# Kernel tuning notes

Hardware: AMD Instinct MI355X
Metric: run time of the kernel (lower is better)

Reference implementation:

```python
import jax, jax.numpy as jnp
import numpy as np

N_HEADS = 16


def setup_inputs() -> dict:
    key = jax.random.key(0)
    ks = jax.random.split(key, 6)
    b, s, d = 1, 2048, 2048
    x = jax.random.normal(ks[0], (b, s, d), dtype=jnp.float32)
    Wqkv = jax.random.normal(ks[1], (d, 3 * d), dtype=jnp.float32) * (d ** -0.5)
    Wqkv_bias = jax.random.normal(ks[2], (3 * d,), dtype=jnp.float32) * 0.02
    out_w = jax.random.normal(ks[3], (d, d), dtype=jnp.float32) * (d ** -0.5)
    out_b = jax.random.normal(ks[4], (d,), dtype=jnp.float32) * 0.02
    attn_bias = jax.random.normal(ks[5], (1, N_HEADS, 1, s), dtype=jnp.float32)
    key_padding_mask = jnp.ones((b, s), dtype=bool)
    return {"x": x, "Wqkv": Wqkv, "Wqkv_bias": Wqkv_bias, "out_w": out_w,
            "out_b": out_b, "attn_bias": attn_bias,
            "key_padding_mask": key_padding_mask}


def reference(x, Wqkv, Wqkv_bias, out_w, out_b, attn_bias, key_padding_mask):
    b, s, d = x.shape
    h = N_HEADS
    dh = d // h
    qkv = x @ Wqkv + Wqkv_bias                      # [b, s, 3d]
    q, k, v = jnp.split(qkv, 3, axis=-1)
    q = q.reshape(b, s, h, dh).transpose(0, 2, 1, 3)  # b h s d
    k = k.reshape(b, s, h, dh).transpose(0, 2, 1, 3)
    v = v.reshape(b, s, h, dh).transpose(0, 2, 1, 3)
    scale = 1.0 / jnp.sqrt(jnp.asarray(dh, x.dtype))
    attn_weight = jnp.einsum('bhqd,bhkd->bhqk', q, k) * scale
    attn_weight = attn_weight + attn_bias           # broadcast [1,h,1,s]
    min_val = jnp.finfo(x.dtype).min
    # key padding mask: [b, s_k] -> [b,1,1,s_k]
    attn_weight = jnp.where(key_padding_mask[:, None, None, :], attn_weight, min_val)
    # causal mask (s_q == s_k)
    causal = jnp.tril(jnp.ones((s, s), dtype=bool))
    attn_weight = jnp.where(causal[None, None, :, :], attn_weight, min_val)
    attn_weight = jax.nn.softmax(attn_weight, axis=-1)
    out = jnp.einsum('bhqk,bhkd->bhqd', attn_weight, v)
    out = out.transpose(0, 2, 1, 3).reshape(b, s, d)  # b s (h d)
    return out @ out_w + out_b
```

## Files before the change

### kernel.cpp

```cpp
#include <hip/hip_runtime.h>
#include <hip/hip_bf16.h>
#include <stdint.h>


#define SQ 2048
#define DM 2048
#define NH 16
#define DH 128
#define N3 6144
#define QKVN (NH * SQ * DH)

typedef unsigned short u16;
typedef __bf16 bf16_t;
typedef bf16_t bf16x8 __attribute__((ext_vector_type(8)));
typedef float f32x4 __attribute__((ext_vector_type(4)));
typedef const __attribute__((address_space(1))) unsigned int guint;
typedef __attribute__((address_space(3))) unsigned int luint;

__device__ __forceinline__ float b2f(u16 u) {
    union { uint32_t i; float f; } c; c.i = ((uint32_t)u) << 16; return c.f;
}
__device__ __forceinline__ u16 f2b(float f) {
    union { float f; uint32_t i; } c; c.f = f;
    uint32_t r = c.i + 0x7FFF + ((c.i >> 16) & 1);
    return (u16)(r >> 16);
}
__device__ __forceinline__ uint32_t pk(u16 a, u16 b) {
    return (uint32_t)a | ((uint32_t)b << 16);
}
__device__ __forceinline__ uint32_t pkrnd(float a, float b) {
    union { float f; uint32_t i; } x, y; x.f = a; y.f = b;
    return __builtin_amdgcn_perm(y.i + 0x8000u, x.i + 0x8000u, 0x07060302u);
}
__device__ __forceinline__ float ld1(const void* p, size_t i, bool fp32) {
    return fp32 ? ((const float*)p)[i] : b2f(((const u16*)p)[i]);
}

__global__ void detect_dtype(const void* x, int* flag) {
    __shared__ int bad;
    if (threadIdx.x == 0) bad = 0;
    __syncthreads();
    float v = b2f(((const u16*)x)[threadIdx.x]);
    if (!(fabsf(v) <= 1024.0f)) atomicOr(&bad, 1);
    __syncthreads();
    if (threadIdx.x == 0) *flag = bad;
}

__global__ __launch_bounds__(256) void convert_x(
    const void* __restrict__ x, u16* __restrict__ xb, const int* __restrict__ flagp)
{
    const bool fp32 = (*flagp != 0);
    const size_t i = ((size_t)blockIdx.x * 256 + threadIdx.x) * 8;
    uint4 v;
    if (fp32) {
        const float* p = (const float*)x + i;
        float4 a = *(const float4*)p, b = *(const float4*)(p + 4);
        v.x = pkrnd(a.x, a.y); v.y = pkrnd(a.z, a.w);
        v.z = pkrnd(b.x, b.y); v.w = pkrnd(b.z, b.w);
    } else {
        v = *(const uint4*)((const u16*)x + i);
    }
    *(uint4*)(xb + i) = v;
}

__global__ __launch_bounds__(256) void transpose_w(
    const void* __restrict__ W, u16* __restrict__ Wt, int N,
    const int* __restrict__ flagp)
{
    const bool fp32 = (*flagp != 0);
    __shared__ __attribute__((aligned(16))) u16 tile[64 * 72];
    const int t = threadIdx.x;
    const int n0 = blockIdx.x * 64, k0 = blockIdx.y * 64;
#pragma unroll
    for (int i = 0; i < 2; ++i) {
        int c = t + 256 * i; int kr = c >> 3; int n8 = (c & 7) * 8;
        uint4 v;
        if (fp32) {
            const float* p = (const float*)W + (size_t)(k0 + kr) * N + n0 + n8;
            float4 a = *(const float4*)p, b = *(const float4*)(p + 4);
            v.x = pkrnd(a.x, a.y); v.y = pkrnd(a.z, a.w);
            v.z = pkrnd(b.x, b.y); v.w = pkrnd(b.z, b.w);
        } else {
            v = *(const uint4*)((const u16*)W + (size_t)(k0 + kr) * N + n0 + n8);
        }
        *(uint4*)&tile[kr * 72 + n8] = v;
    }
    __syncthreads();
#pragma unroll
    for (int i = 0; i < 2; ++i) {
        int c = t + 256 * i; int nr = c >> 3; int k8 = (c & 7) * 8;
        uint32_t dw[4];
#pragma unroll
        for (int j = 0; j < 4; ++j)
            dw[j] = pk(tile[(k8 + 2*j) * 72 + nr], tile[(k8 + 2*j + 1) * 72 + nr]);
        *(uint4*)&Wt[(size_t)(n0 + nr) * 2048 + k0 + k8] =
            make_uint4(dw[0], dw[1], dw[2], dw[3]);
    }
}

__global__ __launch_bounds__(256, 2) void qkv_gemm4(
    const u16* __restrict__ xb, const u16* __restrict__ Wt,
    const void* __restrict__ bias,
    u16* __restrict__ Q, u16* __restrict__ K, u16* __restrict__ Vt,
    const int* __restrict__ flagp)
{
    const bool fp32 = (*flagp != 0);
    __shared__ __attribute__((aligned(16))) u16 Alds[2][128 * 64];
    __shared__ __attribute__((aligned(16))) u16 Blds[2][192 * 64];
    const int t = threadIdx.x;
    const int w = t >> 6, l = t & 63;
    const int wm = w >> 1, wn = w & 1;
    const int lq = l & 15, quad = l >> 4;
    const int rsub = t >> 3;
    const int sw = ((t & 7) ^ (rsub & 7)) << 3;

    const int orig = blockIdx.x;
    const int xcd = orig & 7, j = orig >> 3;
    const int bx = (xcd & 3) * 8 + (j & 7);
    const int by = (xcd >> 2) * 8 + (j >> 3);
    const int m0 = by * 128, n0 = bx * 192;

    const u16* Ag = xb + (size_t)m0 * 2048;
    const u16* Bg = Wt + (size_t)n0 * 2048;

#define STAGE_A(u) do {                                                       \
    if ((u) < 32) {                                                           \
      _Pragma("unroll")                                                       \
      for (int i_ = 0; i_ < 4; ++i_) {                                        \
        const int rb_ = i_ * 32;                                              \
        const u16* src_ = Ag + (size_t)(rb_ + rsub) * 2048 + (u) * 64 + sw;   \
        __builtin_amdgcn_global_load_lds((guint*)(const void*)src_,           \
          (luint*)(void*)&Alds[(u) & 1][rb_ * 64 + t * 8], 16, 0, 0);         \
      }                                                                       \
    } } while (0)

#define STAGE_B(u) do {                                                       \
    if ((u) < 32) {                                                           \
      _Pragma("unroll")                                                       \
      for (int i_ = 0; i_ < 6; ++i_) {                                        \
        const int rb_ = i_ * 32;                                              \
        const u16* src_ = Bg + (size_t)(rb_ + rsub) * 2048 + (u) * 64 + sw;   \
        __builtin_amdgcn_global_load_lds((guint*)(const void*)src_,           \
          (luint*)(void*)&Blds[(u) & 1][rb_ * 64 + t * 8], 16, 0, 0);         \
      }                                                                       \
    } } while (0)

#define READ_A(buf, mh) do {                                                  \
    _Pragma("unroll")                                                         \
    for (int mf_ = 0; mf_ < 2; ++mf_) {                                       \
      const int r_ = wm*64 + ((mh)*2 + mf_)*16 + lq;                          \
      _Pragma("unroll")                                                       \
      for (int ks_ = 0; ks_ < 2; ++ks_) {                                     \
        const int c_ = (ks_*4 + quad) ^ (r_ & 7);                             \
        a[(mh)*2 + mf_][ks_] = *(const bf16x8*)&Alds[buf][r_*64 + c_*8];      \
      }                                                                       \
    } } while (0)

#define READ_B(dst, buf, nhh) do {                                            \
    _Pragma("unroll")                                                         \
    for (int nf_ = 0; nf_ < 3; ++nf_) {                                       \
      const int r_ = wn*96 + ((nhh)*3 + nf_)*16 + lq;                         \
      _Pragma("unroll")                                                       \
      for (int ks_ = 0; ks_ < 2; ++ks_) {                                     \
        const int c_ = (ks_*4 + quad) ^ (r_ & 7);                             \
        dst[nf_][ks_] = *(const bf16x8*)&Blds[buf][r_*64 + c_*8];             \
      }                                                                       \
    } } while (0)

#define MMA_Q(mh, nhh, bsrc) do {                                             \
    _Pragma("unroll")                                                         \
    for (int mf_ = 0; mf_ < 2; ++mf_)                                         \
    _Pragma("unroll")                                                         \
    for (int nf_ = 0; nf_ < 3; ++nf_)                                         \
    _Pragma("unroll")                                                         \
    for (int ks_ = 0; ks_ < 2; ++ks_)                                         \
      acc[(mh)*2+mf_][(nhh)*3+nf_] =                                          \
        __builtin_amdgcn_mfma_f32_16x16x32_bf16(a[(mh)*2+mf_][ks_],           \
          bsrc[nf_][ks_], acc[(mh)*2+mf_][(nhh)*3+nf_], 0, 0, 0);             \
    } while (0)

    const f32x4 vzero = {0.f, 0.f, 0.f, 0.f};
    f32x4 acc[4][6];
#pragma unroll
    for (int i = 0; i < 4; ++i)
#pragma unroll
        for (int j2 = 0; j2 < 6; ++j2) acc[i][j2] = vzero;
    bf16x8 a[4][2], b0[3][2], b1[3][2];

    STAGE_A(0); STAGE_B(0);
    asm volatile("s_waitcnt vmcnt(0)" ::: "memory");
    __builtin_amdgcn_s_barrier();

#pragma unroll 1
    for (int T = 0; T < 32; ++T) {
        const int buf = T & 1;
        STAGE_A(T + 1); STAGE_B(T + 1);
        READ_A(buf, 0); READ_A(buf, 1);
        READ_B(b0, buf, 0); READ_B(b1, buf, 1);
        asm volatile("s_waitcnt lgkmcnt(0)" ::: "memory");
        __builtin_amdgcn_s_setprio(1);
        MMA_Q(0, 0, b0); MMA_Q(0, 1, b1);
        MMA_Q(1, 0, b0); MMA_Q(1, 1, b1);
        __builtin_amdgcn_s_setprio(0);
        asm volatile("s_waitcnt vmcnt(0)" ::: "memory");
        __builtin_amdgcn_s_barrier();
    }

    const float scale = 0.08838834764831845f;
#pragma unroll
    for (int nf = 0; nf < 6; ++nf) {
        const int n = n0 + wn*96 + nf*16 + lq;
        const float bn = ld1(bias, n, fp32);
        const int which = n >> 11, r2 = n & 2047, h = r2 >> 7, dc = r2 & 127;
#pragma unroll
        for (int mf = 0; mf < 4; ++mf) {
#pragma unroll
            for (int r = 0; r < 4; ++r) {
                const int m = m0 + wm*64 + mf*16 + quad*4 + r;
                const float val = acc[mf][nf][r] + bn;
                if (which == 0)
                    Q[((size_t)(h << 11) + m) * DH + dc] = f2b(val * scale);
                else if (which == 1)
                    K[((size_t)(h << 11) + m) * DH + dc] = f2b(val);
                else {
                    const int kl = m & 63;
                    const int pos = ((kl >> 5) << 5) + (((kl >> 2) & 3) << 3)
                                  + (((kl >> 4) & 1) << 2) + (kl & 3);
                    const int mp = (m & ~63) | pos;
                    Vt[((size_t)h * DH + dc) * SQ + mp] = f2b(val);
                }
            }
        }
    }
#undef STAGE_A
#undef STAGE_B
#undef READ_A
#undef READ_B
#undef MMA_Q
}

__global__ __launch_bounds__(256) void attn_mfma(
    const u16* __restrict__ Q, const u16* __restrict__ K,
    const u16* __restrict__ Vt, const void* __restrict__ attn_bias,
    u16* __restrict__ Ob0, u16* __restrict__ Ob1,
    float* __restrict__ Lb0, float* __restrict__ Lb1,
    const int* __restrict__ flagp)
{
    const bool fp32 = (*flagp != 0);
    __shared__ __attribute__((aligned(16))) u16 Ks[2][4 * 64 * 32];
    __shared__ __attribute__((aligned(16))) u16 Vs[2][128 * 64];
    __shared__ __attribute__((aligned(16))) float biasF[2048];

    const int t = threadIdx.x;
    const int w = t >> 6, l = t & 63;
    const int lq = l & 15, quad = l >> 4;
    const int px = blockIdx.x, h = blockIdx.y, par = blockIdx.z;

    const u16* Qh = Q + (size_t)h * SQ * DH;
    const u16* Kh = K + (size_t)h * SQ * DH;
    const u16* Vh = Vt + (size_t)h * DH * SQ;
    u16* Ob = par ? Ob1 : Ob0;
    float* Lb = par ? Lb1 : Lb0;

#pragma unroll
    for (int i = 0; i < 8; ++i) {
        int j = t + 256 * i;
        biasF[j] = ld1(attn_bias, (size_t)h * SQ + j, fp32);
    }

#define STAGE_KV(kt_, b_) do {                                                \
    const int k0_ = (kt_) * 64;                                               \
    _Pragma("unroll")                                                         \
    for (int i_ = 0; i_ < 4; ++i_) {                                          \
        const int ci_ = w * 4 + i_;                                           \
        const int kc_ = ci_ >> 2, kg_ = ci_ & 3;                              \
        const u16* srck_ = Kh + (size_t)(k0_ + kg_*16 + (l >> 2)) * DH        \
                         + kc_*32 + (l & 3) * 8;                              \
        __builtin_amdgcn_global_load_lds((guint*)(const void*)srck_,          \
            (luint*)(void*)&Ks[b_][ci_ * 512], 16, 0, 0);                     \
        const int dim_ = ci_ * 8 + (l >> 3);                                  \
        const u16* srcv_ = Vh + (size_t)dim_ * SQ + k0_                       \
                         + (((l & 7) ^ (l >> 3)) << 3);                       \
        __builtin_amdgcn_global_load_lds((guint*)(const void*)srcv_,          \
            (luint*)(void*)&Vs[b_][ci_ * 512], 16, 0, 0);                     \
    } } while (0)

    const f32x4 vzero = {0.f, 0.f, 0.f, 0.f};

    for (int phase = 0; phase < 2; ++phase) {
        const int qt = phase ? (15 - px) : px;
        const int q0 = qt * 128;
        const int qb = q0 + w * 32;

        bf16x8 bq[2][4];
#pragma unroll
        for (int s = 0; s < 2; ++s)
#pragma unroll
            for (int kc = 0; kc < 4; ++kc)
                bq[s][kc] = *(const bf16x8*)(Qh + (size_t)(qb + s*16 + lq) * DH
                                             + kc*32 + quad*8);

        __syncthreads();
        STAGE_KV(par, 0);
        asm volatile("s_waitcnt vmcnt(0)" ::: "memory");
        __builtin_amdgcn_s_barrier();

        f32x4 O[2][8];
#pragma unroll
        for (int s = 0; s < 2; ++s)
#pragma unroll
            for (int i = 0; i < 8; ++i) O[s][i] = vzero;
        float lsum[2] = {0.0f, 0.0f};

        int buf = 0;
        const int ktmax = 2 * qt + 1;
        for (int kt = par; kt <= ktmax; kt += 2) {
            const int k0 = kt * 64;
            if (kt + 2 <= ktmax) STAGE_KV(kt + 2, buf ^ 1);

            f32x4 S[2][4];
#pragma unroll
            for (int s = 0; s < 2; ++s)
#pragma unroll
                for (int ks = 0; ks < 4; ++ks) S[s][ks] = vzero;
#pragma unroll
            for (int kc = 0; kc < 4; ++kc) {
#pragma unroll
                for (int ks = 0; ks < 4; ++ks) {
                    bf16x8 ak = *(const bf16x8*)&Ks[buf][kc*2048 + (ks*16 + lq)*32 + quad*8];
                    S[0][ks] = __builtin_amdgcn_mfma_f32_16x16x32_bf16(ak, bq[0][kc], S[0][ks], 0, 0, 0);
                    S[1][ks] = __builtin_amdgcn_mfma_f32_16x16x32_bf16(ak, bq[1][kc], S[1][ks], 0, 0, 0);
                }
            }

            uint32_t Ppk[2][4][2];
#pragma unroll
            for (int s = 0; s < 2; ++s) {
                const int qbs = qb + s * 16;
                const bool full = (k0 + 63) <= qbs;
                float part = 0.0f;
#pragma unroll
                for (int ks = 0; ks < 4; ++ks) {
                    const f32x4 b4 = *(const f32x4*)&biasF[k0 + ks*16 + quad*4];
                    float p[4];
#pragma unroll
                    for (int r = 0; r < 4; ++r) {
                        float pe = __expf(S[s][ks][r] + b4[r]);
                        if (!full) {
                            const int key = k0 + ks*16 + quad*4 + r;
                            if (key > qbs + lq) pe = 0.0f;
                        }
                        p[r] = pe;
                        part += pe;
                    }
                    Ppk[s][ks][0] = pkrnd(p[0], p[1]);
                    Ppk[s][ks][1] = pkrnd(p[2], p[3]);
                }
                lsum[s] += part;
            }

#pragma unroll
            for (int s2 = 0; s2 < 2; ++s2) {
                union { uint32_t u[4]; bf16x8 v; } bP0, bP1;
                bP0.u[0] = Ppk[0][2*s2][0];   bP0.u[1] = Ppk[0][2*s2][1];
                bP0.u[2] = Ppk[0][2*s2+1][0]; bP0.u[3] = Ppk[0][2*s2+1][1];
                bP1.u[0] = Ppk[1][2*s2][0];   bP1.u[1] = Ppk[1][2*s2][1];
                bP1.u[2] = Ppk[1][2*s2+1][0]; bP1.u[3] = Ppk[1][2*s2+1][1];
                const int ch = ((s2*4 + quad) ^ (lq & 7)) << 3;
#pragma unroll
                for (int ds = 0; ds < 8; ++ds) {
                    bf16x8 aV = *(const bf16x8*)&Vs[buf][(ds*16 + lq)*64 + ch];
                    O[0][ds] = __builtin_amdgcn_mfma_f32_16x16x32_bf16(aV, bP0.v, O[0][ds], 0, 0, 0);
                    O[1][ds] = __builtin_amdgcn_mfma_f32_16x16x32_bf16(aV, bP1.v, O[1][ds], 0, 0, 0);
                }
            }

            asm volatile("s_waitcnt vmcnt(0)" ::: "memory");
            __builtin_amdgcn_s_barrier();
            buf ^= 1;
        }

#pragma unroll
        for (int s = 0; s < 2; ++s) {
            float ls = lsum[s];
            ls += __shfl_xor(ls, 16, 64);
            ls += __shfl_xor(ls, 32, 64);
            if (l < 16) Lb[(size_t)h * SQ + qb + s*16 + l] = ls;
            u16* orow = Ob + (size_t)(qb + s*16 + lq) * DM + h * DH;
#pragma unroll
            for (int ds = 0; ds < 8; ++ds) {
                uint2 o2;
                o2.x = pkrnd(O[s][ds][0], O[s][ds][1]);
                o2.y = pkrnd(O[s][ds][2], O[s][ds][3]);
                *(uint2*)&orow[ds*16 + quad*4] = o2;
            }
        }
    }
#undef STAGE_KV
}

__global__ __launch_bounds__(256) void combine_o(
    const u16* __restrict__ O0, const u16* __restrict__ O1,
    const float* __restrict__ L0, const float* __restrict__ L1,
    u16* __restrict__ attno)
{
    const size_t i = ((size_t)blockIdx.x * 256 + threadIdx.x) * 8;
    const int row = (int)(i >> 11);
    const int h = ((int)i & 2047) >> 7;
    const float inv = 1.0f / (L0[h * SQ + row] + L1[h * SQ + row]);
    const ushort4 a = *(const ushort4*)(O0 + i);
    const ushort4 b = *(const ushort4*)(O1 + i);
    const ushort4 c = *(const ushort4*)(O0 + i + 4);
    const ushort4 d = *(const ushort4*)(O1 + i + 4);
    uint4 v;
    v.x = pkrnd((b2f(a.x)+b2f(b.x))*inv, (b2f(a.y)+b2f(b.y))*inv);
    v.y = pkrnd((b2f(a.z)+b2f(b.z))*inv, (b2f(a.w)+b2f(b.w))*inv);
    v.z = pkrnd((b2f(c.x)+b2f(d.x))*inv, (b2f(c.y)+b2f(d.y))*inv);
    v.w = pkrnd((b2f(c.z)+b2f(d.z))*inv, (b2f(c.w)+b2f(d.w))*inv);
    *(uint4*)(attno + i) = v;
}

__global__ __launch_bounds__(256, 2) void out_gemm(
    const u16* __restrict__ attno, const u16* __restrict__ OWt,
    const void* __restrict__ bias, void* __restrict__ out,
    const int* __restrict__ flagp)
{
    const bool fp32 = (*flagp != 0);
    __shared__ __attribute__((aligned(16))) u16 Alds[2][64 * 64];
    __shared__ __attribute__((aligned(16))) u16 Blds[2][128 * 64];
    const int t = threadIdx.x;
    const int w = t >> 6, l = t & 63;
    const int wm = w >> 1, wn = w & 1;
    const int lq = l & 15, quad = l >> 4;
    const int rsub = t >> 3;
    const int sw = ((t & 7) ^ (rsub & 7)) << 3;

    const int orig = blockIdx.x;
    const int xcd = orig & 7, j = orig >> 3;
    const int bx = (xcd & 3) * 4 + (j & 3);
    const int by = (xcd >> 2) * 16 + (j >> 2);
    const int m0 = by * 64, n0 = bx * 128;

    const u16* Ag = attno + (size_t)m0 * 2048;
    const u16* Bg = OWt + (size_t)n0 * 2048;

#define O_STAGE_A(u) do {                                                     \
    if ((u) < 32) {                                                           \
      _Pragma("unroll")                                                       \
      for (int i_ = 0; i_ < 2; ++i_) {                                        \
        const int rb_ = i_ * 32;                                              \
        const u16* src_ = Ag + (size_t)(rb_ + rsub) * 2048 + (u) * 64 + sw;   \
        __builtin_amdgcn_global_load_lds((guint*)(const void*)src_,           \
          (luint*)(void*)&Alds[(u) & 1][rb_ * 64 + t * 8], 16, 0, 0);         \
      }                                                                       \
    } } while (0)

#define O_STAGE_B(u) do {                                                     \
    if ((u) < 32) {                                                           \
      _Pragma("unroll")                                                       \
      for (int i_ = 0; i_ < 4; ++i_) {                                        \
        const int rb_ = i_ * 32;                                              \
        const u16* src_ = Bg + (size_t)(rb_ + rsub) * 2048 + (u) * 64 + sw;   \
        __builtin_amdgcn_global_load_lds((guint*)(const void*)src_,           \
          (luint*)(void*)&Blds[(u) & 1][rb_ * 64 + t * 8], 16, 0, 0);         \
      }                                                                       \
    } } while (0)

#define O_READ_A(buf, mh) do {                                                \
    const int r_ = wm*32 + (mh)*16 + lq;                                      \
    _Pragma("unroll")                                                         \
    for (int ks_ = 0; ks_ < 2; ++ks_) {                                       \
        const int c_ = (ks_*4 + quad) ^ (r_ & 7);                             \
        a[mh][ks_] = *(const bf16x8*)&Alds[buf][r_*64 + c_*8];                \
    } } while (0)

#define O_READ_B(dst, buf, nhh) do {                                          \
    _Pragma("unroll")                                                         \
    for (int nf_ = 0; nf_ < 2; ++nf_) {                                       \
      const int r_ = wn*64 + ((nhh)*2 + nf_)*16 + lq;                         \
      _Pragma("unroll")                                                       \
      for (int ks_ = 0; ks_ < 2; ++ks_) {                                     \
        const int c_ = (ks_*4 + quad) ^ (r_ & 7);                             \
        dst[nf_][ks_] = *(const bf16x8*)&Blds[buf][r_*64 + c_*8];             \
      }                                                                       \
    } } while (0)

#define O_MMA(mh, nhh, bsrc) do {                                             \
    _Pragma("unroll")                                                         \
    for (int nf_ = 0; nf_ < 2; ++nf_)                                         \
    _Pragma("unroll")                                                         \
    for (int ks_ = 0; ks_ < 2; ++ks_)                                         \
      acc[mh][(nhh)*2+nf_] =                                                  \
        __builtin_amdgcn_mfma_f32_16x16x32_bf16(a[mh][ks_], bsrc[nf_][ks_],   \
          acc[mh][(nhh)*2+nf_], 0, 0, 0);                                     \
    } while (0)

    const f32x4 vzero = {0.f, 0.f, 0.f, 0.f};
    f32x4 acc[2][4];
#pragma unroll
    for (int i = 0; i < 2; ++i)
#pragma unroll
        for (int j2 = 0; j2 < 4; ++j2) acc[i][j2] = vzero;
    bf16x8 a[2][2], b0[2][2], b1[2][2];

    O_STAGE_A(0); O_STAGE_B(0);
    asm volatile("s_waitcnt vmcnt(0)" ::: "memory");
    __builtin_amdgcn_s_barrier();

#pragma unroll 1
    for (int T = 0; T < 32; ++T) {
        const int buf = T & 1;
        O_STAGE_A(T + 1); O_STAGE_B(T + 1);
        O_READ_A(buf, 0); O_READ_A(buf, 1);
        O_READ_B(b0, buf, 0); O_READ_B(b1, buf, 1);
        asm volatile("s_waitcnt lgkmcnt(0)" ::: "memory");
        __builtin_amdgcn_s_setprio(1);
        O_MMA(0, 0, b0); O_MMA(0, 1, b1);
        O_MMA(1, 0, b0); O_MMA(1, 1, b1);
        __builtin_amdgcn_s_setprio(0);
        asm volatile("s_waitcnt vmcnt(0)" ::: "memory");
        __builtin_amdgcn_s_barrier();
    }

#pragma unroll
    for (int nf = 0; nf < 4; ++nf) {
        const int n = n0 + wn*64 + nf*16 + lq;
        const float bn = ld1(bias, n, fp32);
#pragma unroll
        for (int mh = 0; mh < 2; ++mh) {
#pragma unroll
            for (int r = 0; r < 4; ++r) {
                const int m = m0 + wm*32 + mh*16 + quad*4 + r;
                const float v = acc[mh][nf][r] + bn;
                const size_t idx = (size_t)m * DM + n;
                if (fp32) ((float*)out)[idx] = v;
                else      ((u16*)out)[idx]  = f2b(v);
            }
        }
    }
#undef O_STAGE_A
#undef O_STAGE_B
#undef O_READ_A
#undef O_READ_B
#undef O_MMA
}

extern "C" void kernel_launch(void* const* d_in, const int* in_sizes, int n_in,
                              void* d_out, int out_size, void* d_ws, size_t ws_size,
                              hipStream_t stream)
{
    const void* x      = d_in[0];
    const void* wqkv   = d_in[1];
    const void* wqkv_b = d_in[2];
    const void* out_w  = d_in[3];
    const void* out_b  = d_in[4];
    const void* attn_b = d_in[5];

    char* base = (char*)d_ws;
    int* flag = (int*)base;
    u16* xb   = (u16*)(base + 256);
    u16* Wt   = xb + (size_t)SQ * DM;
    u16* Qb   = Wt + (size_t)N3 * DM;
    u16* Kb   = Qb + QKVN;
    u16* Vtb  = Kb + QKVN;
    float* L0 = (float*)(Vtb + QKVN);
    float* L1 = L0 + NH * SQ;
    u16* OWt  = Wt;
    u16* Ob0  = Wt + (size_t)DM * DM;
    u16* Ob1  = Ob0 + (size_t)SQ * DM;
    u16* attno = xb;

    detect_dtype<<<1, 256, 0, stream>>>(x, flag);
    convert_x<<<(SQ * DM) / (256 * 8), 256, 0, stream>>>(x, xb, flag);
    transpose_w<<<dim3(N3/64, DM/64), 256, 0, stream>>>(wqkv, Wt, N3, flag);
    qkv_gemm4<<<dim3(512), 256, 0, stream>>>(xb, Wt, wqkv_b, Qb, Kb, Vtb, flag);
    transpose_w<<<dim3(DM/64, DM/64), 256, 0, stream>>>(out_w, OWt, DM, flag);
    attn_mfma<<<dim3(8, NH, 2), 256, 0, stream>>>(Qb, Kb, Vtb, attn_b,
                                                  Ob0, Ob1, L0, L1, flag);
    combine_o<<<(SQ * DM) / (256 * 8), 256, 0, stream>>>(Ob0, Ob1, L0, L1, attno);
    out_gemm<<<dim3(512), 256, 0, stream>>>(attno, OWt, out_b, d_out, flag);
}
```

Before: 283.9 us.

## Fuse prep kernels and software-pipeline the QKV GEMM with 2-deep prefetch

Merges dtype detection, x conversion and both weight transposes into one prep launch, and moves OWt to its own workspace region so the out_w transpose no longer has to wait for the QKV GEMM. The QKV GEMM main loop is restructured into four sub-phases per K-tile. Each phase interleaves LDS fragment reads, split global-to-LDS staging two tiles ahead, and MFMA bursts, using partial vmcnt waits in place of a full drain every iteration. This aims to hide global-load latency and trim launch overhead, but it adds more barriers and a larger workspace footprint.

```diff
diff --git a/kernel.cpp b/kernel.cpp
--- a/kernel.cpp
+++ b/kernel.cpp
@@ -36,50 +36,63 @@
     return fp32 ? ((const float*)p)[i] : b2f(((const u16*)p)[i]);
 }
 
-__global__ void detect_dtype(const void* x, int* flag) {
+__global__ __launch_bounds__(256) void prep(
+    const void* __restrict__ x, const void* __restrict__ wqkv,
+    const void* __restrict__ out_w,
+    u16* __restrict__ xb, u16* __restrict__ Wt, u16* __restrict__ OWt,
+    int* __restrict__ flag)
+{
     __shared__ int bad;
-    if (threadIdx.x == 0) bad = 0;
-    __syncthreads();
-    float v = b2f(((const u16*)x)[threadIdx.x]);
-    if (!(fabsf(v) <= 1024.0f)) atomicOr(&bad, 1);
-    __syncthreads();
-    if (threadIdx.x == 0) *flag = bad;
-}
-
-__global__ __launch_bounds__(256) void convert_x(
-    const void* __restrict__ x, u16* __restrict__ xb, const int* __restrict__ flagp)
-{
-    const bool fp32 = (*flagp != 0);
-    const size_t i = ((size_t)blockIdx.x * 256 + threadIdx.x) * 8;
-    uint4 v;
-    if (fp32) {
-        const float* p = (const float*)x + i;
-        float4 a = *(const float4*)p, b = *(const float4*)(p + 4);
-        v.x = pkrnd(a.x, a.y); v.y = pkrnd(a.z, a.w);
-        v.z = pkrnd(b.x, b.y); v.w = pkrnd(b.z, b.w);
-    } else {
-        v = *(const uint4*)((const u16*)x + i);
-    }
-    *(uint4*)(xb + i) = v;
-}
-
-__global__ __launch_bounds__(256) void transpose_w(
-    const void* __restrict__ W, u16* __restrict__ Wt, int N,
-    const int* __restrict__ flagp)
-{
-    const bool fp32 = (*flagp != 0);
     __shared__ __attribute__((aligned(16))) u16 tile[64 * 72];
     const int t = threadIdx.x;
-    const int n0 = blockIdx.x * 64, k0 = blockIdx.y * 64;
+    if (t == 0) bad = 0;
+    __syncthreads();
+    {
+        float v = b2f(((const u16*)x)[t]);
+        if (!(fabsf(v) <= 1024.0f)) atomicOr(&bad, 1);
+    }
+    __syncthreads();
+    const bool fp32 = (bad != 0);
+    const int b = blockIdx.x;
+    if (b == 0 && t == 0) *flag = bad;
+
+    if (b < 2048) {
+        const size_t i = ((size_t)b * 256 + t) * 8;
+        uint4 v;
+        if (fp32) {
+            const float* p = (const float*)x + i;
+            float4 a = *(const float4*)p, b4 = *(const float4*)(p + 4);
+            v.x = pkrnd(a.x, a.y);  v.y = pkrnd(a.z, a.w);
+            v.z = pkrnd(b4.x, b4.y); v.w = pkrnd(b4.z, b4.w);
+        } else {
+            v = *(const uint4*)((const u16*)x + i);
+        }
+        *(uint4*)(xb + i) = v;
+        return;
+    }
+
+    const void* W;
+    u16* dst;
+    int N, bx, by;
+    if (b < 5120) {
+        W = wqkv; dst = Wt; N = N3;
+        const int idx = b - 2048;
+        bx = idx % 96; by = idx / 96;
+    } else {
+        W = out_w; dst = OWt; N = DM;
+        const int idx = b - 5120;
+        bx = idx % 32; by = idx / 32;
+    }
+    const int n0 = bx * 64, k0 = by * 64;
 #pragma unroll
     for (int i = 0; i < 2; ++i) {
         int c = t + 256 * i; int kr = c >> 3; int n8 = (c & 7) * 8;
         uint4 v;
         if (fp32) {
             const float* p = (const float*)W + (size_t)(k0 + kr) * N + n0 + n8;
-            float4 a = *(const float4*)p, b = *(const float4*)(p + 4);
-            v.x = pkrnd(a.x, a.y); v.y = pkrnd(a.z, a.w);
-            v.z = pkrnd(b.x, b.y); v.w = pkrnd(b.z, b.w);
+            float4 a = *(const float4*)p, b4 = *(const float4*)(p + 4);
+            v.x = pkrnd(a.x, a.y);  v.y = pkrnd(a.z, a.w);
+            v.z = pkrnd(b4.x, b4.y); v.w = pkrnd(b4.z, b4.w);
         } else {
             v = *(const uint4*)((const u16*)W + (size_t)(k0 + kr) * N + n0 + n8);
         }
@@ -93,7 +106,7 @@
 #pragma unroll
         for (int j = 0; j < 4; ++j)
             dw[j] = pk(tile[(k8 + 2*j) * 72 + nr], tile[(k8 + 2*j + 1) * 72 + nr]);
-        *(uint4*)&Wt[(size_t)(n0 + nr) * 2048 + k0 + k8] =
+        *(uint4*)&dst[(size_t)(n0 + nr) * 2048 + k0 + k8] =
             make_uint4(dw[0], dw[1], dw[2], dw[3]);
     }
 }
@@ -123,11 +136,11 @@
     const u16* Ag = xb + (size_t)m0 * 2048;
     const u16* Bg = Wt + (size_t)n0 * 2048;
 
-#define STAGE_A(u) do {                                                       \
+#define STAGE_A(u, ue) do {                                                   \
     if ((u) < 32) {                                                           \
       _Pragma("unroll")                                                       \
-      for (int i_ = 0; i_ < 4; ++i_) {                                        \
-        const int rb_ = i_ * 32;                                              \
+      for (int i_ = 0; i_ < 2; ++i_) {                                        \
+        const int rb_ = i_ * 64 + (ue) * 32;                                  \
         const u16* src_ = Ag + (size_t)(rb_ + rsub) * 2048 + (u) * 64 + sw;   \
         __builtin_amdgcn_global_load_lds((guint*)(const void*)src_,           \
           (luint*)(void*)&Alds[(u) & 1][rb_ * 64 + t * 8], 16, 0, 0);         \
@@ -152,7 +165,7 @@
       _Pragma("unroll")                                                       \
       for (int ks_ = 0; ks_ < 2; ++ks_) {                                     \
         const int c_ = (ks_*4 + quad) ^ (r_ & 7);                             \
-        a[(mh)*2 + mf_][ks_] = *(const bf16x8*)&Alds[buf][r_*64 + c_*8];      \
+        a[mf_][ks_] = *(const bf16x8*)&Alds[buf][r_*64 + c_*8];               \
       }                                                                       \
     } } while (0)
 
@@ -168,6 +181,7 @@
     } } while (0)
 
 #define MMA_Q(mh, nhh, bsrc) do {                                             \
+    __builtin_amdgcn_s_setprio(1);                                            \
     _Pragma("unroll")                                                         \
     for (int mf_ = 0; mf_ < 2; ++mf_)                                         \
     _Pragma("unroll")                                                         \
@@ -175,9 +189,42 @@
     _Pragma("unroll")                                                         \
     for (int ks_ = 0; ks_ < 2; ++ks_)                                         \
       acc[(mh)*2+mf_][(nhh)*3+nf_] =                                          \
-        __builtin_amdgcn_mfma_f32_16x16x32_bf16(a[(mh)*2+mf_][ks_],           \
-          bsrc[nf_][ks_], acc[(mh)*2+mf_][(nhh)*3+nf_], 0, 0, 0);             \
-    } while (0)
+        __builtin_amdgcn_mfma_f32_16x16x32_bf16(a[mf_][ks_], bsrc[nf_][ks_],  \
+          acc[(mh)*2+mf_][(nhh)*3+nf_], 0, 0, 0);                             \
+    __builtin_amdgcn_s_setprio(0);                                            \
+} while (0)
+
+#define TILE_BODY(T, buf, BEC, BEN) do {                                      \
+                                                                      \
+    READ_A(buf, 0);                                                           \
+    __builtin_amdgcn_s_barrier();                                             \
+    asm volatile("s_waitcnt lgkmcnt(0)" ::: "memory");                        \
+    MMA_Q(0, 0, BEC);                                                         \
+    __builtin_amdgcn_s_barrier();                                             \
+                                                                      \
+    READ_B(bo, buf, 1);                                                       \
+    STAGE_A((T) + 2, 0);                                                      \
+    if ((T) >= 30) asm volatile("s_waitcnt vmcnt(0)" ::: "memory");           \
+    else           asm volatile("s_waitcnt vmcnt(2)" ::: "memory");           \
+    __builtin_amdgcn_s_barrier();                                             \
+    asm volatile("s_waitcnt lgkmcnt(0)" ::: "memory");                        \
+    MMA_Q(0, 1, bo);                                                          \
+    __builtin_amdgcn_s_barrier();                                             \
+                                                                      \
+    READ_A(buf, 1);                                                           \
+    STAGE_B((T) + 2);                                                         \
+    __builtin_amdgcn_s_barrier();                                             \
+    asm volatile("s_waitcnt lgkmcnt(0)" ::: "memory");                        \
+    MMA_Q(1, 1, bo);                                                          \
+    __builtin_amdgcn_s_barrier();                                             \
+                                                                      \
+    READ_B(BEN, (buf) ^ 1, 0);                                                \
+    STAGE_A((T) + 2, 1);                                                      \
+    __builtin_amdgcn_s_barrier();                                             \
+    asm volatile("s_waitcnt lgkmcnt(0)" ::: "memory");                        \
+    MMA_Q(1, 0, BEC);                                                         \
+    __builtin_amdgcn_s_barrier();                                             \
+} while (0)
 
     const f32x4 vzero = {0.f, 0.f, 0.f, 0.f};
     f32x4 acc[4][6];
@@ -185,25 +232,18 @@
     for (int i = 0; i < 4; ++i)
 #pragma unroll
         for (int j2 = 0; j2 < 6; ++j2) acc[i][j2] = vzero;
-    bf16x8 a[4][2], b0[3][2], b1[3][2];
-
-    STAGE_A(0); STAGE_B(0);
-    asm volatile("s_waitcnt vmcnt(0)" ::: "memory");
+    bf16x8 a[2][2], bo[3][2], be_a[3][2], be_b[3][2];
+
+    STAGE_A(0, 0); STAGE_B(0); STAGE_A(0, 1);
+    STAGE_A(1, 0); STAGE_B(1); STAGE_A(1, 1);
+    asm volatile("s_waitcnt vmcnt(10)" ::: "memory");
     __builtin_amdgcn_s_barrier();
+    READ_B(be_a, 0, 0);
 
 #pragma unroll 1
-    for (int T = 0; T < 32; ++T) {
-        const int buf = T & 1;
-        STAGE_A(T + 1); STAGE_B(T + 1);
-        READ_A(buf, 0); READ_A(buf, 1);
-        READ_B(b0, buf, 0); READ_B(b1, buf, 1);
-        asm volatile("s_waitcnt lgkmcnt(0)" ::: "memory");
-        __builtin_amdgcn_s_setprio(1);
-        MMA_Q(0, 0, b0); MMA_Q(0, 1, b1);
-        MMA_Q(1, 0, b0); MMA_Q(1, 1, b1);
-        __builtin_amdgcn_s_setprio(0);
-        asm volatile("s_waitcnt vmcnt(0)" ::: "memory");
-        __builtin_amdgcn_s_barrier();
+    for (int T = 0; T < 32; T += 2) {
+        TILE_BODY(T,     0, be_a, be_b);
+        TILE_BODY(T + 1, 1, be_b, be_a);
     }
 
     const float scale = 0.08838834764831845f;
@@ -237,6 +277,7 @@
 #undef READ_A
 #undef READ_B
 #undef MMA_Q
+#undef TILE_BODY
 }
 
 __global__ __launch_bounds__(256) void attn_mfma(
@@ -565,16 +606,13 @@
     u16* Vtb  = Kb + QKVN;
     float* L0 = (float*)(Vtb + QKVN);
     float* L1 = L0 + NH * SQ;
-    u16* OWt  = Wt;
-    u16* Ob0  = Wt + (size_t)DM * DM;
+    u16* OWt  = (u16*)(L1 + NH * SQ);
+    u16* Ob0  = Wt;
     u16* Ob1  = Ob0 + (size_t)SQ * DM;
     u16* attno = xb;
 
-    detect_dtype<<<1, 256, 0, stream>>>(x, flag);
-    convert_x<<<(SQ * DM) / (256 * 8), 256, 0, stream>>>(x, xb, flag);
-    transpose_w<<<dim3(N3/64, DM/64), 256, 0, stream>>>(wqkv, Wt, N3, flag);
+    prep<<<dim3(6144), 256, 0, stream>>>(x, wqkv, out_w, xb, Wt, OWt, flag);
     qkv_gemm4<<<dim3(512), 256, 0, stream>>>(xb, Wt, wqkv_b, Qb, Kb, Vtb, flag);
-    transpose_w<<<dim3(DM/64, DM/64), 256, 0, stream>>>(out_w, OWt, DM, flag);
     attn_mfma<<<dim3(8, NH, 2), 256, 0, stream>>>(Qb, Kb, Vtb, attn_b,
                                                   Ob0, Ob1, L0, L1, flag);
     combine_o<<<(SQ * DM) / (256 * 8), 256, 0, stream>>>(Ob0, Ob1, L0, L1, attno);
```

Measured after the change: 276.6 us, median of 2. 1.03x faster.
